# Optimization experiments

Measured on AMD Instinct MI355X. Metric: run time of the kernel, lower is better.

The kernel has to match this reference:

```python
import jax, jax.numpy as jnp
import numpy as np

N = 100000   # nodes
E = 1600000  # edges
H = 8        # heads
D = 16       # per-head dim
HD = H * D   # 128 = hidden_dim * num_heads == input_dim
G = 128      # graphs in batch
OUT = 64     # output_dim
EPS = 1e-3   # BatchNorm eps
NEG_SLOPE = 0.2
THRESH = 0.5


def setup_inputs() -> dict:
    key = jax.random.key(0)
    ks = jax.random.split(key, 20)
    rn = lambda k, s: jax.random.normal(k, s, jnp.float32) * 0.1
    return {
        "h": jax.random.normal(ks[0], (N, HD), jnp.float32),
        "src": jax.random.randint(ks[1], (E,), 0, N),
        "dst": jax.random.randint(ks[2], (E,), 0, N),
        "graph_ids": jnp.sort(jax.random.randint(ks[3], (N,), 0, G)),
        # GAT layer 0 params
        "W0": rn(ks[4], (HD, HD)), "al0": rn(ks[5], (H, D)), "ar0": rn(ks[6], (H, D)), "b0": rn(ks[7], (HD,)),
        "g0": jnp.ones((HD,), jnp.float32), "be0": jnp.zeros((HD,), jnp.float32),
        # GAT layer 1 params
        "W1": rn(ks[8], (HD, HD)), "al1": rn(ks[9], (H, D)), "ar1": rn(ks[10], (H, D)), "b1": rn(ks[11], (HD,)),
        "g1": jnp.ones((HD,), jnp.float32), "be1": jnp.zeros((HD,), jnp.float32),
        # MaskLinear prediction head
        "pred_W": rn(ks[12], (OUT, HD)), "pred_b": rn(ks[13], (OUT,)),
        "mask_real": jax.random.uniform(ks[14], (OUT, HD), jnp.float32),
    }


def _gat(h, W, al, ar, b, src, dst):
    # DGL GATConv: fc -> per-node attn halves -> edge LeakyReLU -> segment softmax over dst -> scatter-add
    feat = (h @ W).reshape(N, H, D)                 # [N,H,D]
    el = jnp.sum(feat * al, axis=-1)                # [N,H]
    er = jnp.sum(feat * ar, axis=-1)                # [N,H]
    e = jax.nn.leaky_relu(el[src] + er[dst], NEG_SLOPE)  # [E,H]
    emax = jax.ops.segment_max(e, dst, num_segments=N)   # [N,H]
    ee = jnp.exp(e - emax[dst])
    denom = jax.ops.segment_sum(ee, dst, num_segments=N) # [N,H]
    a = ee / denom[dst]                             # [E,H]
    msg = a[:, :, None] * feat[src]                 # [E,H,D]
    out = jax.ops.segment_sum(msg, dst, num_segments=N)  # [N,H,D]
    return out.reshape(N, HD) + b


def _bn(x, g, be):
    mu = jnp.mean(x, axis=0)
    var = jnp.mean((x - mu) ** 2, axis=0)
    return (x - mu) * jax.lax.rsqrt(var + EPS) * g + be


def reference(h, src, dst, graph_ids, W0, al0, ar0, b0, g0, be0,
              W1, al1, ar1, b1, g1, be1, pred_W, pred_b, mask_real):
    # layer 0: GAT -> BN -> ReLU (no residual)
    h1 = jax.nn.relu(_bn(_gat(h, W0, al0, ar0, b0, src, dst), g0, be0))
    # layer 1: GAT -> BN -> ReLU + residual
    h2 = jax.nn.relu(_bn(_gat(h1, W1, al1, ar1, b1, src, dst), g1, be1)) + h1
    # SumPooling over graphs in the batch
    pooled = jax.ops.segment_sum(h2, graph_ids, num_segments=G)  # [G,HD]
    # MaskLinear with binarized mask (eval path, no dropout)
    mask = (mask_real > THRESH).astype(pooled.dtype)
    return pooled @ (pred_W * mask).T + pred_b  # [G,OUT]
```

## Files before the change

kernel.cpp:

```cpp
#include <hip/hip_runtime.h>
#include <cstdint>

#define N_NODES 100000
#define N_EDGES 1600000
#define H 8
#define D 16
#define HD 128
#define G_GRAPHS 128
#define OUT_DIM 64
#define EPS 1e-3f
#define NEG 0.2f
#define SCAN_BLOCKS 98
#define NBUCK 196
#define BSHIFT 9
#define BCAP 10240
#define MT 64
#define APAD 136
#define NTILES 1563
#define GEMM_GRID 512
#define BNP_ROWS 64
#define WTROWS 144
#define SRCMASK 0x1FFFF

typedef __attribute__((ext_vector_type(8))) short bf16x8;
typedef __attribute__((ext_vector_type(4))) float f32x4;
typedef __attribute__((ext_vector_type(8))) unsigned short u16x8;

__device__ __forceinline__ unsigned short f2bf(float x) {
    unsigned u = __float_as_uint(x);
    unsigned r = (u + 0x7FFFu + ((u >> 16) & 1u)) >> 16;
    return (unsigned short)r;
}
__device__ __forceinline__ float plo(unsigned q) {
    return __uint_as_float(q << 16);
}
__device__ __forceinline__ float phi(unsigned q) {
    return __uint_as_float(q & 0xFFFF0000u);
}
__device__ __forceinline__ unsigned packbf(float a, float b) {
    return (unsigned)f2bf(a) | ((unsigned)f2bf(b) << 16);
}

__global__ void convert_wt(const float* __restrict__ W0, const float* __restrict__ W1,
                           const float* __restrict__ al0, const float* __restrict__ ar0,
                           const float* __restrict__ al1, const float* __restrict__ ar1,
                           unsigned short* __restrict__ Wt0, unsigned short* __restrict__ Wt1,
                           int* __restrict__ bucketCnt, float* __restrict__ pooled,
                           float* __restrict__ sums01) {
    int t = blockIdx.x * blockDim.x + threadIdx.x;
    if (t < NBUCK) bucketCnt[t] = 0;
    if (t < 512) sums01[t] = 0.f;
    for (int i = t; i < G_GRAPHS * HD; i += gridDim.x * blockDim.x) pooled[i] = 0.f;
    if (t < HD * HD) {
        int k = t >> 7, n = t & 127;
        Wt0[n * HD + k] = f2bf(W0[t]);
        Wt1[n * HD + k] = f2bf(W1[t]);
        return;
    }
    int u = t - HD * HD;
    if (u < HD * 16) {
        int k = u >> 4, j = u & 15;
        int h = j & 7;
        const float* a0 = (j < 8) ? al0 : ar0;
        const float* a1 = (j < 8) ? al1 : ar1;
        float s0 = 0.f, s1 = 0.f;
#pragma unroll
        for (int d = 0; d < 16; ++d) {
            s0 += W0[k * HD + h * 16 + d] * a0[h * 16 + d];
            s1 += W1[k * HD + h * 16 + d] * a1[h * 16 + d];
        }
        Wt0[(HD + j) * HD + k] = f2bf(s0);
        Wt1[(HD + j) * HD + k] = f2bf(s1);
    }
}

__global__ __launch_bounds__(256) void bucket_scatter(const int* __restrict__ src,
                                                      const int* __restrict__ dst,
                                                      int* __restrict__ bucketCnt,
                                                      int* __restrict__ pairs) {
    __shared__ int hist[NBUCK];
    __shared__ int cur[NBUCK];
    int t = threadIdx.x;
    if (t < NBUCK) hist[t] = 0;
    __syncthreads();
    int base = blockIdx.x * 4096;
    int s[16], d[16];
#pragma unroll
    for (int k = 0; k < 16; ++k) {
        int e = base + t + k * 256;
        if (e < N_EDGES) {
            s[k] = src[e];
            d[k] = dst[e];
            atomicAdd(&hist[d[k] >> BSHIFT], 1);
        } else {
            d[k] = -1;
        }
    }
    __syncthreads();
    if (t < NBUCK) {
        int c = hist[t];
        cur[t] = (c > 0) ? atomicAdd(&bucketCnt[t], c) : 0;
    }
    __syncthreads();
#pragma unroll
    for (int k = 0; k < 16; ++k) {
        if (d[k] >= 0) {
            int b = d[k] >> BSHIFT;
            int slot = atomicAdd(&cur[b], 1);
            pairs[(size_t)b * BCAP + slot] = ((d[k] & 511) << 17) | s[k];
        }
    }
}

__global__ __launch_bounds__(256) void bucket_count(const int* __restrict__ bucketCnt,
                                                    const int* __restrict__ pairs,
                                                    int* __restrict__ deg) {
    __shared__ int hist[512];
    int b = blockIdx.x, t = threadIdx.x;
    hist[t] = 0;
    hist[t + 256] = 0;
    __syncthreads();
    int cnt = bucketCnt[b];
    int base0 = b << BSHIFT;
    for (int i = t; i < cnt; i += 256) {
        int w = pairs[(size_t)b * BCAP + i];
        atomicAdd(&hist[w >> 17], 1);
    }
    __syncthreads();
    int n0 = base0 + t, n1 = base0 + t + 256;
    if (n0 < N_NODES) deg[n0] = hist[t];
    if (n1 < N_NODES) deg[n1] = hist[t + 256];
}

__global__ __launch_bounds__(256) void scan1(const int* __restrict__ deg,
                                             int* __restrict__ offs,
                                             int* __restrict__ blksum) {
    __shared__ int bufA[256], bufB[256];
    int t = threadIdx.x;
    int base = blockIdx.x * 1024;
    int idx = base + t * 4;
    int v[4];
#pragma unroll
    for (int i = 0; i < 4; ++i) v[i] = (idx + i < N_NODES) ? deg[idx + i] : 0;
    int s = v[0] + v[1] + v[2] + v[3];
    bufA[t] = s;
    __syncthreads();
    int* a = bufA; int* b = bufB;
    for (int off = 1; off < 256; off <<= 1) {
        int val = a[t];
        if (t >= off) val += a[t - off];
        b[t] = val;
        __syncthreads();
        int* c = a; a = b; b = c;
    }
    int excl = a[t] - s;
#pragma unroll
    for (int i = 0; i < 4; ++i) {
        if (idx + i < N_NODES) offs[idx + i] = excl;
        excl += v[i];
    }
    if (t == 255) blksum[blockIdx.x] = a[255];
}

__global__ void scan2(const int* __restrict__ blksum, int* __restrict__ blkoff) {
    __shared__ int bufA[128], bufB[128];
    int t = threadIdx.x;
    int v = (t < SCAN_BLOCKS) ? blksum[t] : 0;
    bufA[t] = v;
    __syncthreads();
    int* a = bufA; int* b = bufB;
    for (int off = 1; off < 128; off <<= 1) {
        int val = a[t];
        if (t >= off) val += a[t - off];
        b[t] = val;
        __syncthreads();
        int* c = a; a = b; b = c;
    }
    if (t < SCAN_BLOCKS) blkoff[t] = a[t] - v;
}

__global__ __launch_bounds__(256) void scan3(int* __restrict__ offs,
                                             const int* __restrict__ blkoff) {
    int base = blockIdx.x * 1024;
    int add = blkoff[blockIdx.x];
#pragma unroll
    for (int i = 0; i < 4; ++i) {
        int idx = base + threadIdx.x + i * 256;
        if (idx < N_NODES) offs[idx] += add;
    }
}

__global__ __launch_bounds__(256) void bucket_place(const int* __restrict__ bucketCnt,
                                                    const int* __restrict__ pairs,
                                                    const int* __restrict__ offs,
                                                    int* __restrict__ csr_src) {
    __shared__ int cur[512];
    int b = blockIdx.x, t = threadIdx.x;
    cur[t] = 0;
    cur[t + 256] = 0;
    __syncthreads();
    int cnt = bucketCnt[b];
    int base0 = b << BSHIFT;
    for (int i = t; i < cnt; i += 256) {
        int w = pairs[(size_t)b * BCAP + i];
        int dl = w >> 17;
        int r = atomicAdd(&cur[dl], 1);
        csr_src[offs[base0 + dl] + r] = w & SRCMASK;
    }
}

template <int MODE>
__global__ __launch_bounds__(256, 2) void gemm_mfma(const void* __restrict__ Xv,
                                                    const unsigned short* __restrict__ Wt,
                                                    unsigned short* __restrict__ Yb,
                                                    float* __restrict__ el,
                                                    float* __restrict__ er,
                                                    int nrows,
                                                    const float* __restrict__ sums,
                                                    const float* __restrict__ gam,
                                                    const float* __restrict__ bet) {
    __shared__ unsigned short As[MT * APAD];
    __shared__ __align__(16) float scs[HD];
    __shared__ __align__(16) float shs[HD];
    int tid = threadIdx.x;
    int wave = tid >> 6, lane = tid & 63;
    int qd = lane >> 4, l16 = lane & 15;

    if (MODE == 1) {
        if (tid < HD) {
            float invN = 1.0f / (float)N_NODES;
            float mu = sums[tid] * invN;
            float rs = rsqrtf(sums[HD + tid] * invN - mu * mu + EPS);
            float sc = rs * gam[tid];
            scs[tid] = sc;
            shs[tid] = bet[tid] - mu * sc;
        }
        __syncthreads();
    }

    bf16x8 bfr[9][4];
#pragma unroll
    for (int nt = 0; nt < 9; ++nt)
#pragma unroll
        for (int kb = 0; kb < 4; ++kb)
            bfr[nt][kb] = *(const bf16x8*)&Wt[(nt * 16 + l16) * HD + kb * 32 + qd * 8];

    int srow = tid >> 2, scol = (tid & 3) * 32;

    for (int t = blockIdx.x; t < NTILES; t += gridDim.x) {
        int rbase = t * MT;
        {
            int gr = rbase + srow;
            u16x8 o[4];
            if (gr < nrows) {
                if (MODE == 0) {
                    const float* X = (const float*)Xv;
#pragma unroll
                    for (int i = 0; i < 4; ++i) {
                        float4 va = *(const float4*)&X[(size_t)gr * HD + scol + i * 8];
                        float4 vb = *(const float4*)&X[(size_t)gr * HD + scol + i * 8 + 4];
                        o[i][0] = f2bf(va.x); o[i][1] = f2bf(va.y);
                        o[i][2] = f2bf(va.z); o[i][3] = f2bf(va.w);
                        o[i][4] = f2bf(vb.x); o[i][5] = f2bf(vb.y);
                        o[i][6] = f2bf(vb.z); o[i][7] = f2bf(vb.w);
                    }
                } else {
                    const unsigned* X32 = (const unsigned*)Xv;
#pragma unroll
                    for (int i = 0; i < 4; ++i) {
                        uint4 u = *(const uint4*)&X32[(size_t)gr * 64 + (scol >> 1) + i * 4];
                        f32x4 sa = *(const f32x4*)&scs[scol + i * 8];
                        f32x4 sb = *(const f32x4*)&scs[scol + i * 8 + 4];
                        f32x4 ha = *(const f32x4*)&shs[scol + i * 8];
                        f32x4 hb = *(const f32x4*)&shs[scol + i * 8 + 4];
                        float z0 = fmaxf(plo(u.x) * sa.x + ha.x, 0.f);
                        float z1 = fmaxf(phi(u.x) * sa.y + ha.y, 0.f);
                        float z2 = fmaxf(plo(u.y) * sa.z + ha.z, 0.f);
                        float z3 = fmaxf(phi(u.y) * sa.w + ha.w, 0.f);
                        float z4 = fmaxf(plo(u.z) * sb.x + hb.x, 0.f);
                        float z5 = fmaxf(phi(u.z) * sb.y + hb.y, 0.f);
                        float z6 = fmaxf(plo(u.w) * sb.z + hb.z, 0.f);
                        float z7 = fmaxf(phi(u.w) * sb.w + hb.w, 0.f);
                        o[i][0] = f2bf(z0); o[i][1] = f2bf(z1);
                        o[i][2] = f2bf(z2); o[i][3] = f2bf(z3);
                        o[i][4] = f2bf(z4); o[i][5] = f2bf(z5);
                        o[i][6] = f2bf(z6); o[i][7] = f2bf(z7);
                    }
                }
            } else {
#pragma unroll
                for (int i = 0; i < 4; ++i) o[i] = (u16x8)0;
            }
#pragma unroll
            for (int i = 0; i < 4; ++i)
                *(u16x8*)&As[srow * APAD + scol + i * 8] = o[i];
        }
        __syncthreads();
        f32x4 acc[9];
#pragma unroll
        for (int nt = 0; nt < 9; ++nt) acc[nt] = (f32x4){0.f, 0.f, 0.f, 0.f};
        bf16x8 afr[4];
#pragma unroll
        for (int kb = 0; kb < 4; ++kb)
            afr[kb] = *(const bf16x8*)&As[(wave * 16 + l16) * APAD + kb * 32 + qd * 8];
#pragma unroll
        for (int nt = 0; nt < 9; ++nt)
#pragma unroll
            for (int kb = 0; kb < 4; ++kb)
                acc[nt] = __builtin_amdgcn_mfma_f32_16x16x32_bf16(afr[kb], bfr[nt][kb], acc[nt], 0, 0, 0);
        int orow = rbase + wave * 16 + qd * 4;
        if (orow + 3 < nrows) {
#pragma unroll
            for (int nt = 0; nt < 8; ++nt)
#pragma unroll
                for (int r = 0; r < 4; ++r)
                    Yb[(size_t)(orow + r) * HD + nt * 16 + l16] = f2bf(acc[nt][r]);
#pragma unroll
            for (int r = 0; r < 4; ++r) {
                float v = acc[8][r];
                if (l16 < 8) el[(orow + r) * 8 + l16] = v;
                else er[(orow + r) * 8 + (l16 - 8)] = v;
            }
        } else {
#pragma unroll
            for (int nt = 0; nt < 8; ++nt)
                for (int r = 0; r < 4; ++r)
                    if (orow + r < nrows)
                        Yb[(size_t)(orow + r) * HD + nt * 16 + l16] = f2bf(acc[nt][r]);
            for (int r = 0; r < 4; ++r) {
                if (orow + r < nrows) {
                    float v = acc[8][r];
                    if (l16 < 8) el[(orow + r) * 8 + l16] = v;
                    else er[(orow + r) * 8 + (l16 - 8)] = v;
                }
            }
        }
        __syncthreads();
    }
}

__global__ __launch_bounds__(256) void gat_node(const int* __restrict__ offs,
                                                const int* __restrict__ deg,
                                                const int* __restrict__ csr_src,
                                                const float* __restrict__ el,
                                                const float* __restrict__ er,
                                                const uint2* __restrict__ featq,
                                                unsigned* __restrict__ gatb) {
    int node = blockIdx.x * 4 + (threadIdx.x >> 6);
    if (node >= N_NODES) return;
    int lane = threadIdx.x & 63;
    int h7 = lane & 7;
    int eidx = lane >> 3;
    int l32 = lane & 31;
    int hacc = l32 >> 2;
    int half = lane >> 5;
    int ibase = half * 8 + hacc;

    int p = offs[node];
    int cnt = deg[node];
    float ern = er[node * 8 + h7];
    float ds = 0.f, a0 = 0.f, a1 = 0.f, a2 = 0.f, a3 = 0.f;

    int nfull = cnt & ~7;
    if (nfull) {
        int s = csr_src[p + eidx];
        float x = el[(unsigned)s * 8u + h7];
        int c = 0;
        for (;;) {
            float v = x + ern;
            v = fmaxf(v, NEG * v);
            float e = __expf(v);
            ds += e;
            int cn = c + 8;
            int snext = 0; float xnext = 0.f;
            if (cn < nfull) {
                snext = csr_src[p + cn + eidx];
                xnext = el[(unsigned)snext * 8u + h7];
            }
#pragma unroll
            for (int k = 0; k < 4; ++k) {
                float ek = __shfl(e, ibase + 16 * k);
                int sk = __shfl(s, ibase + 16 * k);
                uint2 q = featq[(size_t)((unsigned)sk * 32u + (unsigned)l32)];
                a0 += ek * plo(q.x); a1 += ek * phi(q.x);
                a2 += ek * plo(q.y); a3 += ek * phi(q.y);
            }
            if (cn >= nfull) break;
            c = cn; s = snext; x = xnext;
        }
    }
    int rem = cnt & 7;
    if (rem) {
        int s = 0; float e = 0.f;
        if (eidx < rem) {
            s = csr_src[p + nfull + eidx];
            float v = el[(unsigned)s * 8u + h7] + ern;
            v = fmaxf(v, NEG * v);
            e = __expf(v);
        }
        ds += e;
        int nst = (rem + 1) >> 1;
        for (int k = 0; k < nst; ++k) {
            float ek = __shfl(e, ibase + 16 * k);
            int sk = __shfl(s, ibase + 16 * k);
            uint2 q = featq[(size_t)((unsigned)sk * 32u + (unsigned)l32)];
            a0 += ek * plo(q.x); a1 += ek * phi(q.x);
            a2 += ek * plo(q.y); a3 += ek * phi(q.y);
        }
    }
    ds += __shfl_xor(ds, 8);
    ds += __shfl_xor(ds, 16);
    ds += __shfl_xor(ds, 32);
    float dfull = __shfl(ds, hacc);
    float invd = dfull > 0.f ? 1.f / dfull : 0.f;
    a0 += __shfl_xor(a0, 32);
    a1 += __shfl_xor(a1, 32);
    a2 += __shfl_xor(a2, 32);
    a3 += __shfl_xor(a3, 32);
    if (half == 0) {
        uint2 w;
        w.x = packbf(a0 * invd, a1 * invd);
        w.y = packbf(a2 * invd, a3 * invd);
        ((uint2*)gatb)[(size_t)node * 32 + l32] = w;
    }
}

__global__ __launch_bounds__(256) void bn_stats(const unsigned* __restrict__ xb,
                                                float* __restrict__ sums, int nrows) {
    int cp = threadIdx.x & 63;
    int rr = threadIdx.x >> 6;
    float s0 = 0.f, q0 = 0.f, s1 = 0.f, q1 = 0.f;
    for (int r = blockIdx.x * 4 + rr; r < nrows; r += gridDim.x * 4) {
        unsigned u = xb[(size_t)r * 64 + cp];
        float a = plo(u), b = phi(u);
        s0 += a; q0 += a * a;
        s1 += b; q1 += b * b;
    }
    __shared__ float red[4][256];
    red[0][threadIdx.x] = s0;
    red[1][threadIdx.x] = q0;
    red[2][threadIdx.x] = s1;
    red[3][threadIdx.x] = q1;
    __syncthreads();
    if (rr == 0) {
        int c0 = cp * 2, c1 = c0 + 1;
        float ts0 = red[0][cp] + red[0][cp + 64] + red[0][cp + 128] + red[0][cp + 192];
        float tq0 = red[1][cp] + red[1][cp + 64] + red[1][cp + 128] + red[1][cp + 192];
        float ts1 = red[2][cp] + red[2][cp + 64] + red[2][cp + 128] + red[2][cp + 192];
        float tq1 = red[3][cp] + red[3][cp + 64] + red[3][cp + 128] + red[3][cp + 192];
        atomicAdd(&sums[c0], ts0);
        atomicAdd(&sums[128 + c0], tq0);
        atomicAdd(&sums[c1], ts1);
        atomicAdd(&sums[128 + c1], tq1);
    }
}

__global__ __launch_bounds__(256) void bn_pool(const unsigned* __restrict__ gat1,
                                               const float* __restrict__ sums1,
                                               const float* __restrict__ g1v,
                                               const float* __restrict__ be1v,
                                               const unsigned* __restrict__ gat0,
                                               const float* __restrict__ sums0,
                                               const float* __restrict__ g0v,
                                               const float* __restrict__ be0v,
                                               const int* __restrict__ gid,
                                               float* __restrict__ pooled) {
    int cp = threadIdx.x & 63;
    int rr = threadIdx.x >> 6;
    int c0 = cp * 2, c1 = c0 + 1;
    float invN = 1.0f / (float)N_NODES;
    float mu10 = sums1[c0] * invN, mu11 = sums1[c1] * invN;
    float rs10 = rsqrtf(sums1[128 + c0] * invN - mu10 * mu10 + EPS);
    float rs11 = rsqrtf(sums1[128 + c1] * invN - mu11 * mu11 + EPS);
    float A10 = rs10 * g1v[c0], B10 = be1v[c0] - mu10 * A10;
    float A11 = rs11 * g1v[c1], B11 = be1v[c1] - mu11 * A11;
    float mu00 = sums0[c0] * invN, mu01 = sums0[c1] * invN;
    float rs00 = rsqrtf(sums0[128 + c0] * invN - mu00 * mu00 + EPS);
    float rs01 = rsqrtf(sums0[128 + c1] * invN - mu01 * mu01 + EPS);
    float A00 = rs00 * g0v[c0], B00 = be0v[c0] - mu00 * A00;
    float A01 = rs01 * g0v[c1], B01 = be0v[c1] - mu01 * A01;
    int r0 = blockIdx.x * BNP_ROWS;
    int rend = r0 + BNP_ROWS < N_NODES ? r0 + BNP_ROWS : N_NODES;
    int r = r0 + rr;
    if (r >= rend) return;
    float a0 = 0.f, a1 = 0.f;
    int cur = gid[r];
    for (; r < rend; r += 4) {
        int gg = gid[r];
        if (gg != cur) {
            atomicAdd(&pooled[cur * HD + c0], a0);
            atomicAdd(&pooled[cur * HD + c1], a1);
            a0 = a1 = 0.f;
            cur = gg;
        }
        unsigned u = gat1[(size_t)r * 64 + cp];
        float z0 = plo(u) * A10 + B10;
        float z1 = phi(u) * A11 + B11;
        z0 = z0 > 0.f ? z0 : 0.f;
        z1 = z1 > 0.f ? z1 : 0.f;
        unsigned v = gat0[(size_t)r * 64 + cp];
        float h0 = plo(v) * A00 + B00;
        float h1 = phi(v) * A01 + B01;
        h0 = h0 > 0.f ? h0 : 0.f;
        h1 = h1 > 0.f ? h1 : 0.f;
        a0 += z0 + h0;
        a1 += z1 + h1;
    }
    atomicAdd(&pooled[cur * HD + c0], a0);
    atomicAdd(&pooled[cur * HD + c1], a1);
}

__global__ void pred_kernel(const float* __restrict__ pooled, const float* __restrict__ W,
                            const float* __restrict__ b, const float* __restrict__ mask,
                            float* __restrict__ out) {
    int t = blockIdx.x * blockDim.x + threadIdx.x;
    if (t >= G_GRAPHS * OUT_DIM) return;
    int g = t >> 6, o = t & 63;
    float acc = b[o];
#pragma unroll 4
    for (int c = 0; c < HD; ++c) {
        float m = mask[o * HD + c] > 0.5f ? 1.f : 0.f;
        acc += pooled[g * HD + c] * W[o * HD + c] * m;
    }
    out[t] = acc;
}

extern "C" void kernel_launch(void* const* d_in, const int* in_sizes, int n_in,
                              void* d_out, int out_size, void* d_ws, size_t ws_size,
                              hipStream_t stream) {
    const float* h   = (const float*)d_in[0];
    const int*   src = (const int*)d_in[1];
    const int*   dst = (const int*)d_in[2];
    const int*   gid = (const int*)d_in[3];
    const float* W0  = (const float*)d_in[4];
    const float* al0 = (const float*)d_in[5];
    const float* ar0 = (const float*)d_in[6];
    const float* g0  = (const float*)d_in[8];
    const float* be0 = (const float*)d_in[9];
    const float* W1  = (const float*)d_in[10];
    const float* al1 = (const float*)d_in[11];
    const float* ar1 = (const float*)d_in[12];
    const float* g1  = (const float*)d_in[14];
    const float* be1 = (const float*)d_in[15];
    const float* pW  = (const float*)d_in[16];
    const float* pb  = (const float*)d_in[17];
    const float* msk = (const float*)d_in[18];
    float* out = (float*)d_out;

    unsigned short* gat0  = (unsigned short*)d_ws;
    unsigned short* gat1  = gat0 + (size_t)N_NODES * HD;
    unsigned short* featb = gat1 + (size_t)N_NODES * HD;
    float* el   = (float*)(featb + (size_t)N_NODES * HD);
    float* er   = el + (size_t)N_NODES * H;
    int*   offs = (int*)(er + (size_t)N_NODES * H);
    int*   deg  = offs + N_NODES;
    int*   csr_src = deg + N_NODES;
    int*   bucketCnt = csr_src + N_EDGES;
    int*   blksum = bucketCnt + 256;
    int*   blkoff = blksum + 128;
    float* sums0  = (float*)(blkoff + 128);
    float* sums1  = sums0 + 256;
    float* pooled = sums1 + 256;
    unsigned short* wt0 = (unsigned short*)(pooled + G_GRAPHS * HD);
    unsigned short* wt1 = wt0 + WTROWS * HD;
    int*   pairs  = (int*)gat1;

    const int TB = 256;
    dim3 blk(TB);
    int bsc_blocks  = (N_EDGES + 4095) / 4096;
    int node_blocks = (N_NODES + 3) / 4;
    int bnp_blocks  = (N_NODES + BNP_ROWS - 1) / BNP_ROWS;
    int cw_blocks   = (HD * HD + HD * 16 + TB - 1) / TB;

    convert_wt<<<cw_blocks, blk, 0, stream>>>(W0, W1, al0, ar0, al1, ar1, wt0, wt1,
                                              bucketCnt, pooled, sums0);
    bucket_scatter<<<bsc_blocks, blk, 0, stream>>>(src, dst, bucketCnt, pairs);
    bucket_count<<<NBUCK, blk, 0, stream>>>(bucketCnt, pairs, deg);
    scan1<<<SCAN_BLOCKS, blk, 0, stream>>>(deg, offs, blksum);
    scan2<<<1, 128, 0, stream>>>(blksum, blkoff);
    scan3<<<SCAN_BLOCKS, blk, 0, stream>>>(offs, blkoff);
    bucket_place<<<NBUCK, blk, 0, stream>>>(bucketCnt, pairs, offs, csr_src);

    gemm_mfma<0><<<GEMM_GRID, blk, 0, stream>>>(h, wt0, featb, el, er, N_NODES,
                                                nullptr, nullptr, nullptr);
    gat_node<<<node_blocks, blk, 0, stream>>>(offs, deg, csr_src, el, er,
                                              (const uint2*)featb, (unsigned*)gat0);
    bn_stats<<<512, blk, 0, stream>>>((const unsigned*)gat0, sums0, N_NODES);

    gemm_mfma<1><<<GEMM_GRID, blk, 0, stream>>>(gat0, wt1, featb, el, er, N_NODES,
                                                sums0, g0, be0);
    gat_node<<<node_blocks, blk, 0, stream>>>(offs, deg, csr_src, el, er,
                                              (const uint2*)featb, (unsigned*)gat1);
    bn_stats<<<512, blk, 0, stream>>>((const unsigned*)gat1, sums1, N_NODES);
    bn_pool<<<bnp_blocks, blk, 0, stream>>>((const unsigned*)gat1, sums1, g1, be1,
                                            (const unsigned*)gat0, sums0, g0, be0,
                                            gid, pooled);

    pred_kernel<<<(G_GRAPHS * OUT_DIM + TB - 1) / TB, blk, 0, stream>>>(pooled, pW, pb, msk, out);
}
```

Measured before the change: 474.2 us.

## Fuse CSR build count/scan/place into one per-bucket kernel; retile bn_stats

Replaces the bucket_count, three-pass scan and bucket_place kernels with one bucket_finish kernel. Each block scans the bucket counts to find its global base, builds a local degree histogram, scans it in shared memory, and places sources directly into the CSR. This removes four kernel launches and the deg/offs round trips through global memory, at the cost of every block redundantly scanning the 196 bucket counts. bn_stats now gives each block a contiguous chunk of 128 rows instead of grid-striding over 512 blocks, which launches about 782 blocks and issues more atomics.

```diff
diff --git a/kernel.cpp b/kernel.cpp
--- a/kernel.cpp
+++ b/kernel.cpp
@@ -10,7 +10,6 @@
 #define OUT_DIM 64
 #define EPS 1e-3f
 #define NEG 0.2f
-#define SCAN_BLOCKS 98
 #define NBUCK 196
 #define BSHIFT 9
 #define BCAP 10240
@@ -19,6 +18,7 @@
 #define NTILES 1563
 #define GEMM_GRID 512
 #define BNP_ROWS 64
+#define BNS_ROWS 128
 #define WTROWS 144
 #define SRCMASK 0x1FFFF
 
@@ -112,100 +112,66 @@
     }
 }
 
-__global__ __launch_bounds__(256) void bucket_count(const int* __restrict__ bucketCnt,
-                                                    const int* __restrict__ pairs,
-                                                    int* __restrict__ deg) {
+__global__ __launch_bounds__(256) void bucket_finish(const int* __restrict__ bucketCnt,
+                                                     const int* __restrict__ pairs,
+                                                     int* __restrict__ deg,
+                                                     int* __restrict__ offs,
+                                                     int* __restrict__ csr_src) {
     __shared__ int hist[512];
+    __shared__ int loc[512];
+    __shared__ int bufA[256], bufB[256];
+    __shared__ int bbase_sh;
     int b = blockIdx.x, t = threadIdx.x;
+    int mycnt = bucketCnt[b];
+    int base0 = b << BSHIFT;
+
+    bufA[t] = (t < NBUCK) ? bucketCnt[t] : 0;
+    __syncthreads();
+    {
+        int* a = bufA; int* bb = bufB;
+        for (int off = 1; off < 256; off <<= 1) {
+            int val = a[t];
+            if (t >= off) val += a[t - off];
+            bb[t] = val;
+            __syncthreads();
+            int* c = a; a = bb; bb = c;
+        }
+        if (t == 0) bbase_sh = a[b] - mycnt;
+    }
     hist[t] = 0;
     hist[t + 256] = 0;
     __syncthreads();
-    int cnt = bucketCnt[b];
-    int base0 = b << BSHIFT;
-    for (int i = t; i < cnt; i += 256) {
-        int w = pairs[(size_t)b * BCAP + i];
-        atomicAdd(&hist[w >> 17], 1);
-    }
-    __syncthreads();
-    int n0 = base0 + t, n1 = base0 + t + 256;
-    if (n0 < N_NODES) deg[n0] = hist[t];
-    if (n1 < N_NODES) deg[n1] = hist[t + 256];
-}
-
-__global__ __launch_bounds__(256) void scan1(const int* __restrict__ deg,
-                                             int* __restrict__ offs,
-                                             int* __restrict__ blksum) {
-    __shared__ int bufA[256], bufB[256];
-    int t = threadIdx.x;
-    int base = blockIdx.x * 1024;
-    int idx = base + t * 4;
-    int v[4];
-#pragma unroll
-    for (int i = 0; i < 4; ++i) v[i] = (idx + i < N_NODES) ? deg[idx + i] : 0;
-    int s = v[0] + v[1] + v[2] + v[3];
-    bufA[t] = s;
-    __syncthreads();
-    int* a = bufA; int* b = bufB;
-    for (int off = 1; off < 256; off <<= 1) {
-        int val = a[t];
-        if (t >= off) val += a[t - off];
-        b[t] = val;
-        __syncthreads();
-        int* c = a; a = b; b = c;
-    }
-    int excl = a[t] - s;
-#pragma unroll
-    for (int i = 0; i < 4; ++i) {
-        if (idx + i < N_NODES) offs[idx + i] = excl;
-        excl += v[i];
-    }
-    if (t == 255) blksum[blockIdx.x] = a[255];
-}
-
-__global__ void scan2(const int* __restrict__ blksum, int* __restrict__ blkoff) {
-    __shared__ int bufA[128], bufB[128];
-    int t = threadIdx.x;
-    int v = (t < SCAN_BLOCKS) ? blksum[t] : 0;
-    bufA[t] = v;
-    __syncthreads();
-    int* a = bufA; int* b = bufB;
-    for (int off = 1; off < 128; off <<= 1) {
-        int val = a[t];
-        if (t >= off) val += a[t - off];
-        b[t] = val;
-        __syncthreads();
-        int* c = a; a = b; b = c;
-    }
-    if (t < SCAN_BLOCKS) blkoff[t] = a[t] - v;
-}
-
-__global__ __launch_bounds__(256) void scan3(int* __restrict__ offs,
-                                             const int* __restrict__ blkoff) {
-    int base = blockIdx.x * 1024;
-    int add = blkoff[blockIdx.x];
-#pragma unroll
-    for (int i = 0; i < 4; ++i) {
-        int idx = base + threadIdx.x + i * 256;
-        if (idx < N_NODES) offs[idx] += add;
-    }
-}
-
-__global__ __launch_bounds__(256) void bucket_place(const int* __restrict__ bucketCnt,
-                                                    const int* __restrict__ pairs,
-                                                    const int* __restrict__ offs,
-                                                    int* __restrict__ csr_src) {
-    __shared__ int cur[512];
-    int b = blockIdx.x, t = threadIdx.x;
-    cur[t] = 0;
-    cur[t + 256] = 0;
-    __syncthreads();
-    int cnt = bucketCnt[b];
-    int base0 = b << BSHIFT;
-    for (int i = t; i < cnt; i += 256) {
+    for (int i = t; i < mycnt; i += 256)
+        atomicAdd(&hist[pairs[(size_t)b * BCAP + i] >> 17], 1);
+    __syncthreads();
+    int s0 = hist[2 * t], s1 = hist[2 * t + 1];
+    int ps = s0 + s1;
+    bufA[t] = ps;
+    __syncthreads();
+    int total_excl;
+    {
+        int* a = bufA; int* bb = bufB;
+        for (int off = 1; off < 256; off <<= 1) {
+            int val = a[t];
+            if (t >= off) val += a[t - off];
+            bb[t] = val;
+            __syncthreads();
+            int* c = a; a = bb; bb = c;
+        }
+        total_excl = a[t] - ps;
+    }
+    int bbase = bbase_sh;
+    loc[2 * t] = total_excl;
+    loc[2 * t + 1] = total_excl + s0;
+    int n0 = base0 + 2 * t, n1 = base0 + 2 * t + 1;
+    if (n0 < N_NODES) { deg[n0] = s0; offs[n0] = bbase + total_excl; }
+    if (n1 < N_NODES) { deg[n1] = s1; offs[n1] = bbase + total_excl + s0; }
+    __syncthreads();
+    for (int i = t; i < mycnt; i += 256) {
         int w = pairs[(size_t)b * BCAP + i];
         int dl = w >> 17;
-        int r = atomicAdd(&cur[dl], 1);
-        csr_src[offs[base0 + dl] + r] = w & SRCMASK;
+        int r = atomicAdd(&loc[dl], 1);
+        csr_src[bbase + r] = w & SRCMASK;
     }
 }
 
@@ -429,8 +395,10 @@
                                                 float* __restrict__ sums, int nrows) {
     int cp = threadIdx.x & 63;
     int rr = threadIdx.x >> 6;
+    int r0 = blockIdx.x * BNS_ROWS;
+    int rend = r0 + BNS_ROWS < nrows ? r0 + BNS_ROWS : nrows;
     float s0 = 0.f, q0 = 0.f, s1 = 0.f, q1 = 0.f;
-    for (int r = blockIdx.x * 4 + rr; r < nrows; r += gridDim.x * 4) {
+    for (int r = r0 + rr; r < rend; r += 4) {
         unsigned u = xb[(size_t)r * 64 + cp];
         float a = plo(u), b = phi(u);
         s0 += a; q0 += a * a;
@@ -556,9 +524,7 @@
     int*   deg  = offs + N_NODES;
     int*   csr_src = deg + N_NODES;
     int*   bucketCnt = csr_src + N_EDGES;
-    int*   blksum = bucketCnt + 256;
-    int*   blkoff = blksum + 128;
-    float* sums0  = (float*)(blkoff + 128);
+    float* sums0  = (float*)(bucketCnt + 256);
     float* sums1  = sums0 + 256;
     float* pooled = sums1 + 256;
     unsigned short* wt0 = (unsigned short*)(pooled + G_GRAPHS * HD);
@@ -569,29 +535,26 @@
     dim3 blk(TB);
     int bsc_blocks  = (N_EDGES + 4095) / 4096;
     int node_blocks = (N_NODES + 3) / 4;
+    int bns_blocks  = (N_NODES + BNS_ROWS - 1) / BNS_ROWS;
     int bnp_blocks  = (N_NODES + BNP_ROWS - 1) / BNP_ROWS;
     int cw_blocks   = (HD * HD + HD * 16 + TB - 1) / TB;
 
     convert_wt<<<cw_blocks, blk, 0, stream>>>(W0, W1, al0, ar0, al1, ar1, wt0, wt1,
                                               bucketCnt, pooled, sums0);
     bucket_scatter<<<bsc_blocks, blk, 0, stream>>>(src, dst, bucketCnt, pairs);
-    bucket_count<<<NBUCK, blk, 0, stream>>>(bucketCnt, pairs, deg);
-    scan1<<<SCAN_BLOCKS, blk, 0, stream>>>(deg, offs, blksum);
-    scan2<<<1, 128, 0, stream>>>(blksum, blkoff);
-    scan3<<<SCAN_BLOCKS, blk, 0, stream>>>(offs, blkoff);
-    bucket_place<<<NBUCK, blk, 0, stream>>>(bucketCnt, pairs, offs, csr_src);
+    bucket_finish<<<NBUCK, blk, 0, stream>>>(bucketCnt, pairs, deg, offs, csr_src);
 
     gemm_mfma<0><<<GEMM_GRID, blk, 0, stream>>>(h, wt0, featb, el, er, N_NODES,
                                                 nullptr, nullptr, nullptr);
     gat_node<<<node_blocks, blk, 0, stream>>>(offs, deg, csr_src, el, er,
                                               (const uint2*)featb, (unsigned*)gat0);
-    bn_stats<<<512, blk, 0, stream>>>((const unsigned*)gat0, sums0, N_NODES);
+    bn_stats<<<bns_blocks, blk, 0, stream>>>((const unsigned*)gat0, sums0, N_NODES);
 
     gemm_mfma<1><<<GEMM_GRID, blk, 0, stream>>>(gat0, wt1, featb, el, er, N_NODES,
                                                 sums0, g0, be0);
     gat_node<<<node_blocks, blk, 0, stream>>>(offs, deg, csr_src, el, er,
                                               (const uint2*)featb, (unsigned*)gat1);
-    bn_stats<<<512, blk, 0, stream>>>((const unsigned*)gat1, sums1, N_NODES);
+    bn_stats<<<bns_blocks, blk, 0, stream>>>((const unsigned*)gat1, sums1, N_NODES);
     bn_pool<<<bnp_blocks, blk, 0, stream>>>((const unsigned*)gat1, sums1, g1, be1,
                                             (const unsigned*)gat0, sums0, g0, be0,
                                             gid, pooled);
```

Measured after the change: 476.8 us. No clear change (+0.6%).
